# Optimization experiments

Measured on AMD Instinct MI355X. Metric: run time of the kernel, lower is better.

Reference implementation:

```python
import jax, jax.numpy as jnp
import numpy as np

NEG_SLOPE = 0.01
H = 128  # hidden_conv_1 == hidden_conv_2


def leaky(x):
    return jnp.where(x >= 0, x, NEG_SLOPE * x)


def gru_cell(x, h, w_ih, w_hh, b_ih, b_hh):
    # PyTorch GRUCell: gates stacked [r, z, n] along dim 0 of w_ih/w_hh
    gi = x @ w_ih.T + b_ih  # [N, 3H]
    gh = h @ w_hh.T + b_hh
    ir, iz, inn = jnp.split(gi, 3, axis=-1)
    hr, hz, hn = jnp.split(gh, 3, axis=-1)
    r = jax.nn.sigmoid(ir + hr)
    z = jax.nn.sigmoid(iz + hz)
    n = jnp.tanh(inn + r * hn)
    return (1.0 - z) * n + z * h


def gcn_conv(x, w, b, src, dst, num_nodes):
    # PyG GCNConv: add self-loops, symmetric normalization, linear first
    xw = x @ w.T  # [N, H]
    loop = jnp.arange(num_nodes, dtype=src.dtype)
    s = jnp.concatenate([src, loop])
    d = jnp.concatenate([dst, loop])
    deg = jax.ops.segment_sum(jnp.ones_like(d, dtype=x.dtype), d, num_segments=num_nodes)
    dinv = jnp.where(deg > 0, jax.lax.rsqrt(deg), 0.0)
    norm = dinv[s] * dinv[d]  # [E+N]
    msg = xw[s] * norm[:, None]
    out = jax.ops.segment_sum(msg, d, num_segments=num_nodes)
    return out + b


def setup_inputs() -> dict:
    key = jax.random.key(0)
    ks = jax.random.split(key, 24)
    N, E, EL, IN_DIM, OUT_DIM = 100000, 600000, 200000, 128, 2

    def lin(k, fan_in, fan_out):
        k1, k2 = jax.random.split(k)
        bound = 1.0 / np.sqrt(fan_in)
        w = jax.random.uniform(k1, (fan_out, fan_in), minval=-bound, maxval=bound, dtype=jnp.float32)
        b = jax.random.uniform(k2, (fan_out,), minval=-bound, maxval=bound, dtype=jnp.float32)
        return w, b

    w_pre1, b_pre1 = lin(ks[0], IN_DIM, 256)
    w_pre2, b_pre2 = lin(ks[1], 256, H)
    w_c1, b_c1 = lin(ks[2], H, H)
    w_c2, b_c2 = lin(ks[3], H, H)
    w_post, b_post = lin(ks[4], H, OUT_DIM)

    def gru_params(k):
        k1, k2, k3, k4 = jax.random.split(k, 4)
        bound = 1.0 / np.sqrt(H)
        u = lambda kk, shape: jax.random.uniform(kk, shape, minval=-bound, maxval=bound, dtype=jnp.float32)
        return u(k1, (3 * H, H)), u(k2, (3 * H, H)), u(k3, (3 * H,)), u(k4, (3 * H,))

    g1_wih, g1_whh, g1_bih, g1_bhh = gru_params(ks[5])
    g2_wih, g2_whh, g2_bih, g2_bhh = gru_params(ks[6])

    x = jax.random.normal(ks[7], (N, IN_DIM), dtype=jnp.float32)
    edge_index = jax.random.randint(ks[8], (2, E), 0, N, dtype=jnp.int64 if jax.config.jax_enable_x64 else jnp.int32)
    edge_label_index = jax.random.randint(ks[9], (2, EL), 0, N, dtype=edge_index.dtype)
    prev_emb0 = jax.random.normal(ks[10], (N, H), dtype=jnp.float32)
    prev_emb1 = jax.random.normal(ks[11], (N, H), dtype=jnp.float32)

    return {
        'x': x, 'edge_index': edge_index, 'edge_label_index': edge_label_index,
        'prev_emb0': prev_emb0, 'prev_emb1': prev_emb1,
        'w_pre1': w_pre1, 'b_pre1': b_pre1, 'w_pre2': w_pre2, 'b_pre2': b_pre2,
        'w_c1': w_c1, 'b_c1': b_c1, 'w_c2': w_c2, 'b_c2': b_c2,
        'w_post': w_post, 'b_post': b_post,
        'g1_wih': g1_wih, 'g1_whh': g1_whh, 'g1_bih': g1_bih, 'g1_bhh': g1_bhh,
        'g2_wih': g2_wih, 'g2_whh': g2_whh, 'g2_bih': g2_bih, 'g2_bhh': g2_bhh,
    }


def reference(x, edge_index, edge_label_index, prev_emb0, prev_emb1,
              w_pre1, b_pre1, w_pre2, b_pre2, w_c1, b_c1, w_c2, b_c2,
              w_post, b_post, g1_wih, g1_whh, g1_bih, g1_bhh,
              g2_wih, g2_whh, g2_bih, g2_bhh):
    N = x.shape[0]
    src, dst = edge_index[0], edge_index[1]

    # preprocess (dropout p=0.0 -> identity)
    h = leaky(x @ w_pre1.T + b_pre1)
    h = leaky(h @ w_pre2.T + b_pre2)

    # unconditional GRU fuse with previous 0-hop embedding (detached in torch)
    h = jax.lax.stop_gradient(gru_cell(h, prev_emb0, g1_wih, g1_whh, g1_bih, g1_bhh))
    emb0 = h

    h = leaky(gcn_conv(h, w_c1, b_c1, src, dst, N))
    h = jax.lax.stop_gradient(gru_cell(h, prev_emb0, g1_wih, g1_whh, g1_bih, g1_bhh))
    emb1 = h

    h = leaky(gcn_conv(h, w_c2, b_c2, src, dst, N))
    h = jax.lax.stop_gradient(gru_cell(h, prev_emb1, g2_wih, g2_whh, g2_bih, g2_bhh))
    emb2 = h

    # LP head: gather + hadamard + linear + sum
    h_src = h[edge_label_index[0]]
    h_dst = h[edge_label_index[1]]
    logits = jnp.sum((h_src * h_dst) @ w_post.T + b_post, axis=-1)  # [EL]
    return logits, emb0, emb1, emb2
```

## Files before the change

kernel.cpp:

```cpp
#include <hip/hip_runtime.h>
#include <hip/hip_bf16.h>
#include <type_traits>


typedef __bf16 bf16;
typedef __bf16 bf16x8 __attribute__((ext_vector_type(8)));
typedef float  f32x4  __attribute__((ext_vector_type(4)));

#define DEV __device__ __forceinline__

DEV f32x4 mfma16(bf16x8 a, bf16x8 b, f32x4 c) {
    return __builtin_amdgcn_mfma_f32_16x16x32_bf16(a, b, c, 0, 0, 0);
}

DEV bf16x8 load_a8(const float* p) {
    f32x4 lo = *(const f32x4*)p;
    f32x4 hi = *(const f32x4*)(p + 4);
    bf16x8 v;
    v[0] = (bf16)lo[0]; v[1] = (bf16)lo[1]; v[2] = (bf16)lo[2]; v[3] = (bf16)lo[3];
    v[4] = (bf16)hi[0]; v[5] = (bf16)hi[1]; v[6] = (bf16)hi[2]; v[7] = (bf16)hi[3];
    return v;
}
DEV bf16x8 load_a8(const bf16* p) { return *(const bf16x8*)p; }

__global__ void cvt8_kernel(const float* s0, const float* s1, const float* s2, const float* s3,
                            const float* s4, const float* s5, const float* s6, const float* s7,
                            bf16* __restrict__ wb) {
    const int i = blockIdx.x * 256 + threadIdx.x;
    if (i >= 294912) return;
    float v;
    if      (i < 32768)  v = s0[i];
    else if (i < 65536)  v = s1[i - 32768];
    else if (i < 81920)  v = s2[i - 65536];
    else if (i < 98304)  v = s3[i - 81920];
    else if (i < 147456) v = s4[i - 98304];
    else if (i < 196608) v = s5[i - 147456];
    else if (i < 245760) v = s6[i - 196608];
    else                 v = s7[i - 245760];
    wb[i] = (bf16)v;
}

template<int Ci, int Co, bool ACT, bool BIAS, typename AT, typename OT>
__global__ __launch_bounds__(256) void gemm_kernel(
    const AT* __restrict__ A, const bf16* __restrict__ W,
    const float* __restrict__ bias, OT* __restrict__ C, int M)
{
    const int tid  = threadIdx.x;
    const int lane = tid & 63, w = tid >> 6;
    const int lr   = lane & 15, ko = lane >> 4;
    const int rbase = blockIdx.x * 128 + w * 32;

    constexpr int KC = Ci / 32;
    constexpr int NT = Co / 16;

    bf16x8 a[2][KC];
#pragma unroll
    for (int m = 0; m < 2; ++m) {
        long arow = rbase + m * 16 + lr; if (arow > M - 1) arow = M - 1;
#pragma unroll
        for (int kc = 0; kc < KC; ++kc)
            a[m][kc] = load_a8(A + arow * Ci + kc * 32 + ko * 8);
    }

#pragma unroll
    for (int t = 0; t < NT; ++t) {
        f32x4 acc0 = {0.f, 0.f, 0.f, 0.f};
        f32x4 acc1 = {0.f, 0.f, 0.f, 0.f};
        const bf16* wp = W + (long)(t * 16 + lr) * Ci + ko * 8;
#pragma unroll
        for (int kc = 0; kc < KC; ++kc) {
            bf16x8 wf = *(const bf16x8*)(wp + kc * 32);
            acc0 = mfma16(a[0][kc], wf, acc0);
            acc1 = mfma16(a[1][kc], wf, acc1);
        }

        const int col = t * 16 + lr;
        float bv = 0.f;
        if (BIAS) bv = bias[col];
#pragma unroll
        for (int j = 0; j < 4; ++j) {
            const int r0 = rbase + ko * 4 + j;
            if (r0 < M) {
                float v = acc0[j] + bv;
                if (ACT) v = (v >= 0.f) ? v : 0.01f * v;
                C[(long)r0 * Co + col] = (OT)v;
            }
            const int r1 = rbase + 16 + ko * 4 + j;
            if (r1 < M) {
                float v = acc1[j] + bv;
                if (ACT) v = (v >= 0.f) ? v : 0.01f * v;
                C[(long)r1 * Co + col] = (OT)v;
            }
        }
    }
}

template<typename XT>
__global__ __launch_bounds__(256) void gru_kernel(
    const XT* x, const float* __restrict__ hp,
    const bf16* __restrict__ wih, const bf16* __restrict__ whh,
    const float* __restrict__ bih, const float* __restrict__ bhh,
    float* out, int N)
{
    __shared__ bf16 Lw[6][16][128];

    const int tid  = threadIdx.x;
    const int lane = tid & 63, w = tid >> 6;
    const int lr   = lane & 15, ko = lane >> 4;
    const long rbase = (long)blockIdx.x * 64 + w * 16;

    long arow = rbase + lr; if (arow > N - 1) arow = N - 1;
    bf16x8 ax[4], ah[4];
#pragma unroll
    for (int kc = 0; kc < 4; ++kc) {
        ax[kc] = load_a8(x  + arow * 128 + kc * 32 + ko * 8);
        ah[kc] = load_a8(hp + arow * 128 + kc * 32 + ko * 8);
    }

    bf16x8 pre[6];
    auto LDW = [&](int tc) {
#pragma unroll
        for (int i = 0; i < 6; ++i) {
            const int ch  = tid + 256 * i;
            const int g   = ch >> 8, rem = ch & 255;
            const int row = rem >> 4, cc = rem & 15;
            const int scc = cc ^ (row & 7);
            pre[i] = *(const bf16x8*)((g < 3 ? wih : whh)
                + (long)(((g % 3) * 128 + tc * 16 + row) * 128 + scc * 8));
        }
    };
    LDW(0);

    for (int tc = 0; tc < 8; ++tc) {
        __syncthreads();
#pragma unroll
        for (int i = 0; i < 6; ++i) {
            const int ch  = tid + 256 * i;
            const int g   = ch >> 8, rem = ch & 255;
            const int row = rem >> 4, cc = rem & 15;
            *(bf16x8*)(&Lw[g][row][cc * 8]) = pre[i];
        }
        __syncthreads();
        if (tc < 7) LDW(tc + 1);

        const int col = tc * 16 + lr;
        const float br = bih[col]       + bhh[col];
        const float bz = bih[128 + col] + bhh[128 + col];
        const float bi = bih[256 + col];
        const float bh = bhh[256 + col];

        f32x4 ar = {0.f, 0.f, 0.f, 0.f};
        f32x4 az = {0.f, 0.f, 0.f, 0.f};
        f32x4 ai = {0.f, 0.f, 0.f, 0.f};
        f32x4 ag = {0.f, 0.f, 0.f, 0.f};
#pragma unroll
        for (int kc = 0; kc < 4; ++kc) {
            const int cc = (kc * 4 + ko) ^ (lr & 7);
            bf16x8 wr_i = *(const bf16x8*)(&Lw[0][lr][cc * 8]);
            bf16x8 wz_i = *(const bf16x8*)(&Lw[1][lr][cc * 8]);
            bf16x8 wn_i = *(const bf16x8*)(&Lw[2][lr][cc * 8]);
            bf16x8 wr_h = *(const bf16x8*)(&Lw[3][lr][cc * 8]);
            bf16x8 wz_h = *(const bf16x8*)(&Lw[4][lr][cc * 8]);
            bf16x8 wn_h = *(const bf16x8*)(&Lw[5][lr][cc * 8]);
            ar = mfma16(ax[kc], wr_i, ar);
            ar = mfma16(ah[kc], wr_h, ar);
            az = mfma16(ax[kc], wz_i, az);
            az = mfma16(ah[kc], wz_h, az);
            ai = mfma16(ax[kc], wn_i, ai);
            ag = mfma16(ah[kc], wn_h, ag);
        }
#pragma unroll
        for (int j = 0; j < 4; ++j) {
            const long row = rbase + ko * 4 + j;
            if (row < N) {
                const float r = 1.f / (1.f + __expf(-(ar[j] + br)));
                const float z = 1.f / (1.f + __expf(-(az[j] + bz)));
                const float pre_ = (ai[j] + bi) + r * (ag[j] + bh);
                const float n = 1.f - 2.f / (1.f + __expf(2.f * pre_));
                out[row * 128 + col] = (1.f - z) * n + z * hp[row * 128 + col];
            }
        }
    }
}

__global__ __launch_bounds__(256) void gg_kernel(
    const bf16* __restrict__ xwb,
    const int* __restrict__ rowptr, const int* __restrict__ degi,
    const int* __restrict__ csr_src, const float* __restrict__ csr_norm,
    const float* __restrict__ dinv, const float* __restrict__ cbias,
    const float* __restrict__ hp,
    const bf16* __restrict__ wih, const bf16* __restrict__ whh,
    const float* __restrict__ bih, const float* __restrict__ bhh,
    float* __restrict__ out, int N)
{
    __shared__ bf16 Lw[6][16][128];

    const int tid  = threadIdx.x;
    const int lane = tid & 63, w = tid >> 6;
    const int lr   = lane & 15, ko = lane >> 4;
    const long rbase = (long)blockIdx.x * 64 + w * 16;

    long arow = rbase + lr; if (arow > N - 1) arow = N - 1;

    float acc[4][8];
#pragma unroll
    for (int kc = 0; kc < 4; ++kc)
#pragma unroll
        for (int j = 0; j < 8; ++j) acc[kc][j] = 0.f;
    {
        const int start = rowptr[arow];
        const int deg   = degi[arow];
        const bf16* xb  = xwb + ko * 8;
        for (int k = 0; k < deg; ++k) {
            const int   s  = csr_src[start + k];
            const float nm = csr_norm[start + k];
            const bf16* vp = xb + (long)s * 128;
            bf16x8 v0 = *(const bf16x8*)(vp);
            bf16x8 v1 = *(const bf16x8*)(vp + 32);
            bf16x8 v2 = *(const bf16x8*)(vp + 64);
            bf16x8 v3 = *(const bf16x8*)(vp + 96);
#pragma unroll
            for (int j = 0; j < 8; ++j) {
                acc[0][j] += (float)v0[j] * nm;
                acc[1][j] += (float)v1[j] * nm;
                acc[2][j] += (float)v2[j] * nm;
                acc[3][j] += (float)v3[j] * nm;
            }
        }
    }

    bf16x8 ax[4], ah[4];
    {
        const float di = dinv[arow], sl = di * di;
        const bf16* vp = xwb + (long)arow * 128 + ko * 8;
#pragma unroll
        for (int kc = 0; kc < 4; ++kc) {
            bf16x8 vd = *(const bf16x8*)(vp + kc * 32);
#pragma unroll
            for (int j = 0; j < 8; ++j) {
                float t = acc[kc][j] + (float)vd[j] * sl + cbias[kc * 32 + ko * 8 + j];
                t = (t >= 0.f) ? t : 0.01f * t;
                ax[kc][j] = (bf16)t;
            }
            ah[kc] = load_a8(hp + arow * 128 + kc * 32 + ko * 8);
        }
    }

    bf16x8 pre[6];
    auto LDW = [&](int tc) {
#pragma unroll
        for (int i = 0; i < 6; ++i) {
            const int ch  = tid + 256 * i;
            const int g   = ch >> 8, rem = ch & 255;
            const int row = rem >> 4, cc = rem & 15;
            const int scc = cc ^ (row & 7);
            pre[i] = *(const bf16x8*)((g < 3 ? wih : whh)
                + (long)(((g % 3) * 128 + tc * 16 + row) * 128 + scc * 8));
        }
    };
    LDW(0);

    for (int tc = 0; tc < 8; ++tc) {
        __syncthreads();
#pragma unroll
        for (int i = 0; i < 6; ++i) {
            const int ch  = tid + 256 * i;
            const int g   = ch >> 8, rem = ch & 255;
            const int row = rem >> 4, cc = rem & 15;
            *(bf16x8*)(&Lw[g][row][cc * 8]) = pre[i];
        }
        __syncthreads();
        if (tc < 7) LDW(tc + 1);

        const int col = tc * 16 + lr;
        const float br = bih[col]       + bhh[col];
        const float bz = bih[128 + col] + bhh[128 + col];
        const float bi = bih[256 + col];
        const float bh = bhh[256 + col];

        f32x4 ar = {0.f, 0.f, 0.f, 0.f};
        f32x4 az = {0.f, 0.f, 0.f, 0.f};
        f32x4 ai = {0.f, 0.f, 0.f, 0.f};
        f32x4 ag = {0.f, 0.f, 0.f, 0.f};
#pragma unroll
        for (int kc = 0; kc < 4; ++kc) {
            const int cc = (kc * 4 + ko) ^ (lr & 7);
            bf16x8 wr_i = *(const bf16x8*)(&Lw[0][lr][cc * 8]);
            bf16x8 wz_i = *(const bf16x8*)(&Lw[1][lr][cc * 8]);
            bf16x8 wn_i = *(const bf16x8*)(&Lw[2][lr][cc * 8]);
            bf16x8 wr_h = *(const bf16x8*)(&Lw[3][lr][cc * 8]);
            bf16x8 wz_h = *(const bf16x8*)(&Lw[4][lr][cc * 8]);
            bf16x8 wn_h = *(const bf16x8*)(&Lw[5][lr][cc * 8]);
            ar = mfma16(ax[kc], wr_i, ar);
            ar = mfma16(ah[kc], wr_h, ar);
            az = mfma16(ax[kc], wz_i, az);
            az = mfma16(ah[kc], wz_h, az);
            ai = mfma16(ax[kc], wn_i, ai);
            ag = mfma16(ah[kc], wn_h, ag);
        }
#pragma unroll
        for (int j = 0; j < 4; ++j) {
            const long row = rbase + ko * 4 + j;
            if (row < N) {
                const float r = 1.f / (1.f + __expf(-(ar[j] + br)));
                const float z = 1.f / (1.f + __expf(-(az[j] + bz)));
                const float pre_ = (ai[j] + bi) + r * (ag[j] + bh);
                const float n = 1.f - 2.f / (1.f + __expf(2.f * pre_));
                out[row * 128 + col] = (1.f - z) * n + z * hp[row * 128 + col];
            }
        }
    }
}

__global__ void deg_kernel(const int* __restrict__ dst, int* degi, int E) {
    const int e = blockIdx.x * 256 + threadIdx.x;
    if (e < E) atomicAdd(&degi[dst[e]], 1);
}
__global__ void scan1_kernel(const int* __restrict__ degi, int* __restrict__ inc,
                             int* __restrict__ bsum, float* __restrict__ dinv, int N) {
    __shared__ int s[256];
    const int i = blockIdx.x * 256 + threadIdx.x;
    const int d = (i < N) ? degi[i] : 0;
    if (i < N) dinv[i] = rsqrtf((float)d + 1.0f);
    s[threadIdx.x] = d;
    __syncthreads();
#pragma unroll
    for (int off = 1; off < 256; off <<= 1) {
        int t = (threadIdx.x >= off) ? s[threadIdx.x - off] : 0;
        __syncthreads();
        s[threadIdx.x] += t;
        __syncthreads();
    }
    if (i < N) inc[i] = s[threadIdx.x];
    if (threadIdx.x == 255) bsum[blockIdx.x] = s[255];
}
__global__ void scan2_kernel(int* bsum, int nb) {
    __shared__ int s[512];
    __shared__ int carry;
    if (threadIdx.x == 0) carry = 0;
    __syncthreads();
    for (int base = 0; base < nb; base += 512) {
        const int i = base + threadIdx.x;
        s[threadIdx.x] = (i < nb) ? bsum[i] : 0;
        __syncthreads();
#pragma unroll
        for (int off = 1; off < 512; off <<= 1) {
            int t = (threadIdx.x >= off) ? s[threadIdx.x - off] : 0;
            __syncthreads();
            s[threadIdx.x] += t;
            __syncthreads();
        }
        const int c = carry;
        if (i < nb) bsum[i] = s[threadIdx.x] + c;
        __syncthreads();
        if (threadIdx.x == 511) carry = c + s[511];
        __syncthreads();
    }
}
__global__ void scan3_kernel(const int* __restrict__ inc, const int* __restrict__ degi,
                             const int* __restrict__ bsum, int* __restrict__ rowptr,
                             int* __restrict__ rp2, int N) {
    const int i = blockIdx.x * 256 + threadIdx.x;
    if (i >= N) return;
    const int prev = (blockIdx.x > 0) ? bsum[blockIdx.x - 1] : 0;
    const int rp = prev + inc[i] - degi[i];
    rowptr[i] = rp;
    rp2[i]    = rp;
}
__global__ void fill_kernel(const int* __restrict__ src, const int* __restrict__ dst,
                            int* rp2, const float* __restrict__ dinv,
                            int* __restrict__ csr_src, float* __restrict__ csr_norm, int E) {
    const int e = blockIdx.x * 256 + threadIdx.x;
    if (e >= E) return;
    const int s = src[e], d = dst[e];
    const int pos = atomicAdd(&rp2[d], 1);
    csr_src[pos]  = s;
    csr_norm[pos] = dinv[s] * dinv[d];
}

template<typename OT>
__global__ __launch_bounds__(256) void gather_kernel(
    const bf16* __restrict__ xwb,
    const int* __restrict__ rowptr, const int* __restrict__ degi,
    const int* __restrict__ csr_src, const float* __restrict__ csr_norm,
    const float* __restrict__ dinv, const float* __restrict__ bias,
    OT* __restrict__ out, int N, int colbase, int cw, int lg)
{
    const long tid = (long)blockIdx.x * 256 + threadIdx.x;
    const long d = tid >> lg;
    const int  c = (int)(tid & ((1 << lg) - 1));
    if (d >= N) return;

    const int start = rowptr[d];
    const int deg   = degi[d];
    const int h     = deg >> 1;
    const bf16* xb  = xwb + c * 8;

    float acca[8] = {0.f, 0.f, 0.f, 0.f, 0.f, 0.f, 0.f, 0.f};
    float accb[8] = {0.f, 0.f, 0.f, 0.f, 0.f, 0.f, 0.f, 0.f};
    for (int k = 0; k < h; ++k) {
        const int   sa = csr_src[start + k];
        const int   sb = csr_src[start + h + k];
        const float na = csr_norm[start + k];
        const float nb_ = csr_norm[start + h + k];
        bf16x8 va = *(const bf16x8*)(xb + (long)sa * cw);
        bf16x8 vb = *(const bf16x8*)(xb + (long)sb * cw);
#pragma unroll
        for (int j = 0; j < 8; ++j) {
            acca[j] += (float)va[j] * na;
            accb[j] += (float)vb[j] * nb_;
        }
    }
    if (deg & 1) {
        const int   s  = csr_src[start + deg - 1];
        const float nm = csr_norm[start + deg - 1];
        bf16x8 v = *(const bf16x8*)(xb + (long)s * cw);
#pragma unroll
        for (int j = 0; j < 8; ++j) acca[j] += (float)v[j] * nm;
    }

    const float di = dinv[d], sl = di * di;
    bf16x8 vd = *(const bf16x8*)(xb + d * cw);
    const int col = colbase + c * 8;
    float v[8];
#pragma unroll
    for (int j = 0; j < 8; ++j) {
        float t = acca[j] + accb[j] + (float)vd[j] * sl + bias[col + j];
        v[j] = (t >= 0.f) ? t : 0.01f * t;
    }
    if constexpr (std::is_same<OT, bf16>::value) {
        bf16x8 o;
#pragma unroll
        for (int j = 0; j < 8; ++j) o[j] = (bf16)v[j];
        *(bf16x8*)(out + d * 128 + col) = o;
    } else {
        f32x4 o0, o1;
#pragma unroll
        for (int j = 0; j < 4; ++j) { o0[j] = v[j]; o1[j] = v[4 + j]; }
        *(f32x4*)(out + d * 128 + col)     = o0;
        *(f32x4*)(out + d * 128 + col + 4) = o1;
    }
}

__global__ __launch_bounds__(256) void lp_kernel(
    const float* __restrict__ emb, const int* __restrict__ eli,
    const float* __restrict__ wpost, const float* __restrict__ bpost,
    float* __restrict__ logits, int EL)
{
    const long t = (long)blockIdx.x * 256 + threadIdx.x;
    const long e = t >> 4;
    const int  c = (int)(t & 15);
    if (e >= EL) return;
    const long s = eli[e], d = eli[EL + e];

    f32x4 a0 = *(const f32x4*)(emb + s * 128 + c * 8);
    f32x4 a1 = *(const f32x4*)(emb + s * 128 + c * 8 + 4);
    f32x4 b0 = *(const f32x4*)(emb + d * 128 + c * 8);
    f32x4 b1 = *(const f32x4*)(emb + d * 128 + c * 8 + 4);
    f32x4 w00 = *(const f32x4*)(wpost + c * 8);
    f32x4 w01 = *(const f32x4*)(wpost + c * 8 + 4);
    f32x4 w10 = *(const f32x4*)(wpost + 128 + c * 8);
    f32x4 w11 = *(const f32x4*)(wpost + 128 + c * 8 + 4);

    float acc = 0.f;
#pragma unroll
    for (int i = 0; i < 4; ++i) {
        acc += a0[i] * b0[i] * (w00[i] + w10[i]);
        acc += a1[i] * b1[i] * (w01[i] + w11[i]);
    }
#pragma unroll
    for (int m = 1; m < 16; m <<= 1) acc += __shfl_xor(acc, m);
    if (c == 0) logits[e] = acc + bpost[0] + bpost[1];
}

extern "C" void kernel_launch(void* const* d_in, const int* in_sizes, int n_in,
                              void* d_out, int out_size, void* d_ws, size_t ws_size,
                              hipStream_t stream) {
    const float* x      = (const float*)d_in[0];
    const int*   ei     = (const int*)d_in[1];
    const int*   eli    = (const int*)d_in[2];
    const float* prev0  = (const float*)d_in[3];
    const float* prev1  = (const float*)d_in[4];
    const float* w_pre1 = (const float*)d_in[5];
    const float* b_pre1 = (const float*)d_in[6];
    const float* w_pre2 = (const float*)d_in[7];
    const float* b_pre2 = (const float*)d_in[8];
    const float* w_c1   = (const float*)d_in[9];
    const float* b_c1   = (const float*)d_in[10];
    const float* w_c2   = (const float*)d_in[11];
    const float* b_c2   = (const float*)d_in[12];
    const float* w_post = (const float*)d_in[13];
    const float* b_post = (const float*)d_in[14];
    const float* g1_wih = (const float*)d_in[15];
    const float* g1_whh = (const float*)d_in[16];
    const float* g1_bih = (const float*)d_in[17];
    const float* g1_bhh = (const float*)d_in[18];
    const float* g2_wih = (const float*)d_in[19];
    const float* g2_whh = (const float*)d_in[20];
    const float* g2_bih = (const float*)d_in[21];
    const float* g2_bhh = (const float*)d_in[22];

    const int N  = in_sizes[0] / 128;
    const int E  = in_sizes[1] / 2;
    const int EL = in_sizes[2] / 2;
    const long NH = (long)N * 128;

    float* out    = (float*)d_out;
    float* logits = out;
    float* emb0   = out + EL;
    float* emb1   = emb0 + NH;
    float* emb2   = emb1 + NH;

    bf16* H1b = (bf16*)emb1;
    bf16* H2b = (bf16*)emb2;
    bf16* h1b = (bf16*)emb2;

    char* ws = (char*)d_ws;
    size_t p = 0;
    auto alloc = [&](size_t bytes) { size_t o = p; p = (p + bytes + 255) & ~(size_t)255; return o; };
    float* dinv    = (float*)(ws + alloc((size_t)N * 4));
    int*   degi    = (int*)  (ws + alloc((size_t)N * 4));
    int*   inc     = (int*)  (ws + alloc((size_t)N * 4));
    int*   rowptr  = (int*)  (ws + alloc((size_t)N * 4));
    int*   rp2     = (int*)  (ws + alloc((size_t)N * 4));
    int*   bsum    = (int*)  (ws + alloc(4096));
    bf16*  wb      = (bf16*) (ws + alloc((size_t)294912 * 2));
    int*   csr_src = (int*)  (ws + alloc((size_t)E * 4));
    float* csr_nrm = (float*)(ws + alloc((size_t)E * 4));
    const size_t fixed = p;
    bf16*  xwb     = (bf16*)(ws + fixed);

    int cw = 128;
    while (cw > 16 && fixed + (size_t)N * cw * 2 > ws_size) cw >>= 1;
    const int lg = __builtin_ctz(cw >> 3);
    const int passes = 128 / cw;
    const bool fused = (cw == 128);
    const bool big_ws = fused &&
        (ws_size >= fixed + (size_t)N * 128 * 2 + (size_t)N * 128 * 2);
    bf16* h2b = big_ws ? (bf16*)(ws + fixed + (size_t)N * 128 * 2) : nullptr;

    bf16* wb_pre1 = wb;
    bf16* wb_pre2 = wb_pre1 + 32768;
    bf16* wb_c1   = wb_pre2 + 32768;
    bf16* wb_c2   = wb_c1 + 16384;
    bf16* wb_g1i  = wb_c2 + 16384;
    bf16* wb_g1h  = wb_g1i + 49152;
    bf16* wb_g2i  = wb_g1h + 49152;
    bf16* wb_g2h  = wb_g2i + 49152;

    const int gB = 256;
    const dim3 blk(gB);
    const int grid_rows128 = (N + 127) / 128;
    const int grid_gru     = (N + 63) / 64;
    const int grid_E       = (E + gB - 1) / gB;
    const int nb           = (N + 255) / 256;

    cvt8_kernel<<<(294912 + 255) / 256, blk, 0, stream>>>(
        w_pre1, w_pre2, w_c1, w_c2, g1_wih, g1_whh, g2_wih, g2_whh, wb);

    hipMemsetAsync(degi, 0, (size_t)N * 4, stream);
    deg_kernel<<<grid_E, blk, 0, stream>>>(ei + E, degi, E);
    scan1_kernel<<<nb, blk, 0, stream>>>(degi, inc, bsum, dinv, N);
    scan2_kernel<<<1, 512, 0, stream>>>(bsum, nb);
    scan3_kernel<<<nb, blk, 0, stream>>>(inc, degi, bsum, rowptr, rp2, N);
    fill_kernel<<<grid_E, blk, 0, stream>>>(ei, ei + E, rp2, dinv, csr_src, csr_nrm, E);

    gemm_kernel<128, 256, true, true, float, bf16><<<grid_rows128, blk, 0, stream>>>(x, wb_pre1, b_pre1, H1b, N);
    gemm_kernel<256, 128, true, true, bf16,  bf16><<<grid_rows128, blk, 0, stream>>>(H1b, wb_pre2, b_pre2, H2b, N);

    gru_kernel<bf16><<<grid_gru, blk, 0, stream>>>(H2b, prev0, wb_g1i, wb_g1h, g1_bih, g1_bhh, emb0, N);

    auto run_gemm = [&](const float* hin, const bf16* wp) {
        switch (cw) {
        case 128: gemm_kernel<128, 128, false, false, float, bf16><<<grid_rows128, blk, 0, stream>>>(hin, wp, nullptr, xwb, N); break;
        case 64:  gemm_kernel<128, 64,  false, false, float, bf16><<<grid_rows128, blk, 0, stream>>>(hin, wp, nullptr, xwb, N); break;
        case 32:  gemm_kernel<128, 32,  false, false, float, bf16><<<grid_rows128, blk, 0, stream>>>(hin, wp, nullptr, xwb, N); break;
        default:  gemm_kernel<128, 16,  false, false, float, bf16><<<grid_rows128, blk, 0, stream>>>(hin, wp, nullptr, xwb, N); break;
        }
    };

    if (fused) {
        run_gemm(emb0, wb_c1);
        gg_kernel<<<grid_gru, blk, 0, stream>>>(xwb, rowptr, degi, csr_src, csr_nrm,
                                                dinv, b_c1, prev0,
                                                wb_g1i, wb_g1h, g1_bih, g1_bhh, emb1, N);
        run_gemm(emb1, wb_c2);
        gg_kernel<<<grid_gru, blk, 0, stream>>>(xwb, rowptr, degi, csr_src, csr_nrm,
                                                dinv, b_c2, prev1,
                                                wb_g2i, wb_g2h, g2_bih, g2_bhh, emb2, N);
    } else {
        const int grid_ga = (int)((((long)N << lg) + gB - 1) / gB);
        for (int ps = 0; ps < passes; ++ps) {
            run_gemm(emb0, wb_c1 + (size_t)(ps * cw) * 128);
            gather_kernel<bf16><<<grid_ga, blk, 0, stream>>>(xwb, rowptr, degi, csr_src, csr_nrm,
                                                             dinv, b_c1, h1b, N, ps * cw, cw, lg);
        }
        gru_kernel<bf16><<<grid_gru, blk, 0, stream>>>(h1b, prev0, wb_g1i, wb_g1h, g1_bih, g1_bhh, emb1, N);
        for (int ps = 0; ps < passes; ++ps) {
            run_gemm(emb1, wb_c2 + (size_t)(ps * cw) * 128);
            if (big_ws)
                gather_kernel<bf16><<<grid_ga, blk, 0, stream>>>(xwb, rowptr, degi, csr_src, csr_nrm,
                                                                 dinv, b_c2, h2b, N, ps * cw, cw, lg);
            else
                gather_kernel<float><<<grid_ga, blk, 0, stream>>>(xwb, rowptr, degi, csr_src, csr_nrm,
                                                                  dinv, b_c2, emb2, N, ps * cw, cw, lg);
        }
        if (big_ws)
            gru_kernel<bf16><<<grid_gru, blk, 0, stream>>>(h2b, prev1, wb_g2i, wb_g2h, g2_bih, g2_bhh, emb2, N);
        else
            gru_kernel<float><<<grid_gru, blk, 0, stream>>>(emb2, prev1, wb_g2i, wb_g2h, g2_bih, g2_bhh, emb2, N);
    }

    lp_kernel<<<(int)(((long)EL * 16 + gB - 1) / gB), blk, 0, stream>>>(emb2, eli, w_post, b_post, logits, EL);
}
```

Measured before the change: 533.9 us.

## Distribute block's CSR edges across all threads with LDS atomic accumulation

The fused gather+GRU kernel no longer gives each lane one destination row to walk serially over its neighbours. All 256 threads now share the block's contiguous edge range, one (edge, 16-byte chunk) pair per thread, and scatter into a shared float accumulator with LDS atomics. This needs a new csr_dst array written by the fill kernel and a rowptr[N] sentinel. The aim is to remove load imbalance and idle lanes from varying degrees, at the cost of LDS atomics, extra shared memory reused for the weight tiles, and extra global traffic for csr_dst.

```diff
diff --git a/kernel.cpp b/kernel.cpp
--- a/kernel.cpp
+++ b/kernel.cpp
@@ -185,64 +185,70 @@
 
 __global__ __launch_bounds__(256) void gg_kernel(
     const bf16* __restrict__ xwb,
-    const int* __restrict__ rowptr, const int* __restrict__ degi,
+    const int* __restrict__ rowptr,
     const int* __restrict__ csr_src, const float* __restrict__ csr_norm,
+    const int* __restrict__ csr_dst,
     const float* __restrict__ dinv, const float* __restrict__ cbias,
     const float* __restrict__ hp,
     const bf16* __restrict__ wih, const bf16* __restrict__ whh,
     const float* __restrict__ bih, const float* __restrict__ bhh,
     float* __restrict__ out, int N)
 {
-    __shared__ bf16 Lw[6][16][128];
+    __shared__ float hacc[64][132];
+    bf16* LwBuf = (bf16*)&hacc[0][0];
 
     const int tid  = threadIdx.x;
     const int lane = tid & 63, w = tid >> 6;
     const int lr   = lane & 15, ko = lane >> 4;
-    const long rbase = (long)blockIdx.x * 64 + w * 16;
-
-    long arow = rbase + lr; if (arow > N - 1) arow = N - 1;
-
-    float acc[4][8];
-#pragma unroll
-    for (int kc = 0; kc < 4; ++kc)
-#pragma unroll
-        for (int j = 0; j < 8; ++j) acc[kc][j] = 0.f;
+    const long rbase = (long)blockIdx.x * 64;
+    const long wrow0 = rbase + w * 16;
+
+    long arow = wrow0 + lr; if (arow > N - 1) arow = N - 1;
+    const int lrow = (int)(arow - rbase);
+
+    float* hf = &hacc[0][0];
+#pragma unroll
+    for (int i = 0; i < 33; ++i) hf[tid + 256 * i] = 0.f;
+
+    bf16x8 ah[4], vd[4];
+#pragma unroll
+    for (int kc = 0; kc < 4; ++kc) {
+        ah[kc] = load_a8(hp + arow * 128 + kc * 32 + ko * 8);
+        vd[kc] = *(const bf16x8*)(xwb + (long)arow * 128 + kc * 32 + ko * 8);
+    }
+    __syncthreads();
+
     {
-        const int start = rowptr[arow];
-        const int deg   = degi[arow];
-        const bf16* xb  = xwb + ko * 8;
-        for (int k = 0; k < deg; ++k) {
-            const int   s  = csr_src[start + k];
-            const float nm = csr_norm[start + k];
-            const bf16* vp = xb + (long)s * 128;
-            bf16x8 v0 = *(const bf16x8*)(vp);
-            bf16x8 v1 = *(const bf16x8*)(vp + 32);
-            bf16x8 v2 = *(const bf16x8*)(vp + 64);
-            bf16x8 v3 = *(const bf16x8*)(vp + 96);
-#pragma unroll
-            for (int j = 0; j < 8; ++j) {
-                acc[0][j] += (float)v0[j] * nm;
-                acc[1][j] += (float)v1[j] * nm;
-                acc[2][j] += (float)v2[j] * nm;
-                acc[3][j] += (float)v3[j] * nm;
-            }
-        }
-    }
-
-    bf16x8 ax[4], ah[4];
+        const int estart = rowptr[rbase];
+        long rend = rbase + 64; if (rend > N) rend = N;
+        const int eend = rowptr[rend];
+        const int npair = (eend - estart) << 4;
+        for (int pi = tid; pi < npair; pi += 256) {
+            const int e = estart + (pi >> 4);
+            const int c = pi & 15;
+            const int   s  = csr_src[e];
+            const float nm = csr_norm[e];
+            const int   r  = csr_dst[e] - (int)rbase;
+            bf16x8 v = *(const bf16x8*)(xwb + (long)s * 128 + c * 8);
+            float* hq = &hacc[r][c * 8];
+#pragma unroll
+            for (int j = 0; j < 8; ++j) atomicAdd(hq + j, (float)v[j] * nm);
+        }
+    }
+    __syncthreads();
+
+    bf16x8 ax[4];
     {
         const float di = dinv[arow], sl = di * di;
-        const bf16* vp = xwb + (long)arow * 128 + ko * 8;
 #pragma unroll
         for (int kc = 0; kc < 4; ++kc) {
-            bf16x8 vd = *(const bf16x8*)(vp + kc * 32);
+            const int c0 = kc * 32 + ko * 8;
 #pragma unroll
             for (int j = 0; j < 8; ++j) {
-                float t = acc[kc][j] + (float)vd[j] * sl + cbias[kc * 32 + ko * 8 + j];
+                float t = hacc[lrow][c0 + j] + (float)vd[kc][j] * sl + cbias[c0 + j];
                 t = (t >= 0.f) ? t : 0.01f * t;
                 ax[kc][j] = (bf16)t;
             }
-            ah[kc] = load_a8(hp + arow * 128 + kc * 32 + ko * 8);
         }
     }
 
@@ -267,7 +273,7 @@
             const int ch  = tid + 256 * i;
             const int g   = ch >> 8, rem = ch & 255;
             const int row = rem >> 4, cc = rem & 15;
-            *(bf16x8*)(&Lw[g][row][cc * 8]) = pre[i];
+            *(bf16x8*)(LwBuf + g * 2048 + row * 128 + cc * 8) = pre[i];
         }
         __syncthreads();
         if (tc < 7) LDW(tc + 1);
@@ -285,12 +291,12 @@
 #pragma unroll
         for (int kc = 0; kc < 4; ++kc) {
             const int cc = (kc * 4 + ko) ^ (lr & 7);
-            bf16x8 wr_i = *(const bf16x8*)(&Lw[0][lr][cc * 8]);
-            bf16x8 wz_i = *(const bf16x8*)(&Lw[1][lr][cc * 8]);
-            bf16x8 wn_i = *(const bf16x8*)(&Lw[2][lr][cc * 8]);
-            bf16x8 wr_h = *(const bf16x8*)(&Lw[3][lr][cc * 8]);
-            bf16x8 wz_h = *(const bf16x8*)(&Lw[4][lr][cc * 8]);
-            bf16x8 wn_h = *(const bf16x8*)(&Lw[5][lr][cc * 8]);
+            bf16x8 wr_i = *(const bf16x8*)(LwBuf + 0 * 2048 + lr * 128 + cc * 8);
+            bf16x8 wz_i = *(const bf16x8*)(LwBuf + 1 * 2048 + lr * 128 + cc * 8);
+            bf16x8 wn_i = *(const bf16x8*)(LwBuf + 2 * 2048 + lr * 128 + cc * 8);
+            bf16x8 wr_h = *(const bf16x8*)(LwBuf + 3 * 2048 + lr * 128 + cc * 8);
+            bf16x8 wz_h = *(const bf16x8*)(LwBuf + 4 * 2048 + lr * 128 + cc * 8);
+            bf16x8 wn_h = *(const bf16x8*)(LwBuf + 5 * 2048 + lr * 128 + cc * 8);
             ar = mfma16(ax[kc], wr_i, ar);
             ar = mfma16(ah[kc], wr_h, ar);
             az = mfma16(ax[kc], wz_i, az);
@@ -300,7 +306,7 @@
         }
 #pragma unroll
         for (int j = 0; j < 4; ++j) {
-            const long row = rbase + ko * 4 + j;
+            const long row = wrow0 + ko * 4 + j;
             if (row < N) {
                 const float r = 1.f / (1.f + __expf(-(ar[j] + br)));
                 const float z = 1.f / (1.f + __expf(-(az[j] + bz)));
@@ -366,16 +372,19 @@
     const int rp = prev + inc[i] - degi[i];
     rowptr[i] = rp;
     rp2[i]    = rp;
+    if (i == N - 1) rowptr[N] = rp + degi[i];
 }
 __global__ void fill_kernel(const int* __restrict__ src, const int* __restrict__ dst,
                             int* rp2, const float* __restrict__ dinv,
-                            int* __restrict__ csr_src, float* __restrict__ csr_norm, int E) {
+                            int* __restrict__ csr_src, float* __restrict__ csr_norm,
+                            int* __restrict__ csr_dst, int E) {
     const int e = blockIdx.x * 256 + threadIdx.x;
     if (e >= E) return;
     const int s = src[e], d = dst[e];
     const int pos = atomicAdd(&rp2[d], 1);
     csr_src[pos]  = s;
     csr_norm[pos] = dinv[s] * dinv[d];
+    csr_dst[pos]  = d;
 }
 
 template<typename OT>
@@ -521,12 +530,13 @@
     float* dinv    = (float*)(ws + alloc((size_t)N * 4));
     int*   degi    = (int*)  (ws + alloc((size_t)N * 4));
     int*   inc     = (int*)  (ws + alloc((size_t)N * 4));
-    int*   rowptr  = (int*)  (ws + alloc((size_t)N * 4));
+    int*   rowptr  = (int*)  (ws + alloc((size_t)(N + 1) * 4));
     int*   rp2     = (int*)  (ws + alloc((size_t)N * 4));
     int*   bsum    = (int*)  (ws + alloc(4096));
     bf16*  wb      = (bf16*) (ws + alloc((size_t)294912 * 2));
     int*   csr_src = (int*)  (ws + alloc((size_t)E * 4));
     float* csr_nrm = (float*)(ws + alloc((size_t)E * 4));
+    int*   csr_dst = (int*)  (ws + alloc((size_t)E * 4));
     const size_t fixed = p;
     bf16*  xwb     = (bf16*)(ws + fixed);
 
@@ -563,7 +573,7 @@
     scan1_kernel<<<nb, blk, 0, stream>>>(degi, inc, bsum, dinv, N);
     scan2_kernel<<<1, 512, 0, stream>>>(bsum, nb);
     scan3_kernel<<<nb, blk, 0, stream>>>(inc, degi, bsum, rowptr, rp2, N);
-    fill_kernel<<<grid_E, blk, 0, stream>>>(ei, ei + E, rp2, dinv, csr_src, csr_nrm, E);
+    fill_kernel<<<grid_E, blk, 0, stream>>>(ei, ei + E, rp2, dinv, csr_src, csr_nrm, csr_dst, E);
 
     gemm_kernel<128, 256, true, true, float, bf16><<<grid_rows128, blk, 0, stream>>>(x, wb_pre1, b_pre1, H1b, N);
     gemm_kernel<256, 128, true, true, bf16,  bf16><<<grid_rows128, blk, 0, stream>>>(H1b, wb_pre2, b_pre2, H2b, N);
@@ -581,11 +591,11 @@
 
     if (fused) {
         run_gemm(emb0, wb_c1);
-        gg_kernel<<<grid_gru, blk, 0, stream>>>(xwb, rowptr, degi, csr_src, csr_nrm,
+        gg_kernel<<<grid_gru, blk, 0, stream>>>(xwb, rowptr, csr_src, csr_nrm, csr_dst,
                                                 dinv, b_c1, prev0,
                                                 wb_g1i, wb_g1h, g1_bih, g1_bhh, emb1, N);
         run_gemm(emb1, wb_c2);
-        gg_kernel<<<grid_gru, blk, 0, stream>>>(xwb, rowptr, degi, csr_src, csr_nrm,
+        gg_kernel<<<grid_gru, blk, 0, stream>>>(xwb, rowptr, csr_src, csr_nrm, csr_dst,
                                                 dinv, b_c2, prev1,
                                                 wb_g2i, wb_g2h, g2_bih, g2_bhh, emb2, N);
     } else {
```

Result: slower. 1.317 ms (+146.6%).

## Sort nodes by in-degree so fused gather-GRU waves have uniform trip counts

Applied to the files above, without the earlier changes.

Adds a degree histogram, scan and scatter that build a permutation of nodes bucketed by in-degree (capped at 63). The fused gather+GRU kernel then processes rows through this permutation, so lanes in a wavefront walk neighbor lists of similar length instead of waiting on the longest row. The cost is three extra small kernels plus a memset, indirect row indexing that scatters the output writes and hp reads, and loss of contiguous access to the prev-embedding rows.

```diff
diff --git a/kernel.cpp b/kernel.cpp
--- a/kernel.cpp
+++ b/kernel.cpp
@@ -187,6 +187,7 @@
     const bf16* __restrict__ xwb,
     const int* __restrict__ rowptr, const int* __restrict__ degi,
     const int* __restrict__ csr_src, const float* __restrict__ csr_norm,
+    const int* __restrict__ perm,
     const float* __restrict__ dinv, const float* __restrict__ cbias,
     const float* __restrict__ hp,
     const bf16* __restrict__ wih, const bf16* __restrict__ whh,
@@ -194,13 +195,21 @@
     float* __restrict__ out, int N)
 {
     __shared__ bf16 Lw[6][16][128];
+    __shared__ int  sperm[64];
 
     const int tid  = threadIdx.x;
     const int lane = tid & 63, w = tid >> 6;
     const int lr   = lane & 15, ko = lane >> 4;
-    const long rbase = (long)blockIdx.x * 64 + w * 16;
-
-    long arow = rbase + lr; if (arow > N - 1) arow = N - 1;
+    const long rbase = (long)blockIdx.x * 64;
+    const long wrow0 = rbase + w * 16;
+
+    if (tid < 64) {
+        long ii = rbase + tid; if (ii > N - 1) ii = N - 1;
+        sperm[tid] = perm[ii];
+    }
+    __syncthreads();
+
+    const long arow = sperm[w * 16 + lr];
 
     float acc[4][8];
 #pragma unroll
@@ -300,8 +309,8 @@
         }
 #pragma unroll
         for (int j = 0; j < 4; ++j) {
-            const long row = rbase + ko * 4 + j;
-            if (row < N) {
+            if (wrow0 + ko * 4 + j < N) {
+                const long row = sperm[w * 16 + ko * 4 + j];
                 const float r = 1.f / (1.f + __expf(-(ar[j] + br)));
                 const float z = 1.f / (1.f + __expf(-(az[j] + bz)));
                 const float pre_ = (ai[j] + bi) + r * (ag[j] + bh);
@@ -366,6 +375,7 @@
     const int rp = prev + inc[i] - degi[i];
     rowptr[i] = rp;
     rp2[i]    = rp;
+    if (i == N - 1) rowptr[N] = rp + degi[i];
 }
 __global__ void fill_kernel(const int* __restrict__ src, const int* __restrict__ dst,
                             int* rp2, const float* __restrict__ dinv,
@@ -376,6 +386,38 @@
     const int pos = atomicAdd(&rp2[d], 1);
     csr_src[pos]  = s;
     csr_norm[pos] = dinv[s] * dinv[d];
+}
+
+__global__ void dhist_kernel(const int* __restrict__ degi, int* dhist, int N) {
+    const int i = blockIdx.x * 256 + threadIdx.x;
+    if (i < N) {
+        int b = degi[i]; if (b > 63) b = 63;
+        atomicAdd(&dhist[b], 1);
+    }
+}
+__global__ void dscan_kernel(int* dhist) {
+    __shared__ int s[64];
+    const int t = threadIdx.x;
+    const int orig = dhist[t];
+    s[t] = orig;
+    __syncthreads();
+#pragma unroll
+    for (int off = 1; off < 64; off <<= 1) {
+        int v = (t >= off) ? s[t - off] : 0;
+        __syncthreads();
+        s[t] += v;
+        __syncthreads();
+    }
+    dhist[t] = s[t] - orig;
+}
+__global__ void dscatter_kernel(const int* __restrict__ degi, int* dhist,
+                                int* __restrict__ perm, int N) {
+    const int i = blockIdx.x * 256 + threadIdx.x;
+    if (i < N) {
+        int b = degi[i]; if (b > 63) b = 63;
+        const int pos = atomicAdd(&dhist[b], 1);
+        perm[pos] = i;
+    }
 }
 
 template<typename OT>
@@ -521,9 +563,11 @@
     float* dinv    = (float*)(ws + alloc((size_t)N * 4));
     int*   degi    = (int*)  (ws + alloc((size_t)N * 4));
     int*   inc     = (int*)  (ws + alloc((size_t)N * 4));
-    int*   rowptr  = (int*)  (ws + alloc((size_t)N * 4));
+    int*   rowptr  = (int*)  (ws + alloc((size_t)(N + 1) * 4));
     int*   rp2     = (int*)  (ws + alloc((size_t)N * 4));
+    int*   perm    = (int*)  (ws + alloc((size_t)N * 4));
     int*   bsum    = (int*)  (ws + alloc(4096));
+    int*   dhist   = (int*)  (ws + alloc(256));
     bf16*  wb      = (bf16*) (ws + alloc((size_t)294912 * 2));
     int*   csr_src = (int*)  (ws + alloc((size_t)E * 4));
     float* csr_nrm = (float*)(ws + alloc((size_t)E * 4));
@@ -553,6 +597,7 @@
     const int grid_rows128 = (N + 127) / 128;
     const int grid_gru     = (N + 63) / 64;
     const int grid_E       = (E + gB - 1) / gB;
+    const int grid_N       = (N + gB - 1) / gB;
     const int nb           = (N + 255) / 256;
 
     cvt8_kernel<<<(294912 + 255) / 256, blk, 0, stream>>>(
@@ -564,6 +609,10 @@
     scan2_kernel<<<1, 512, 0, stream>>>(bsum, nb);
     scan3_kernel<<<nb, blk, 0, stream>>>(inc, degi, bsum, rowptr, rp2, N);
     fill_kernel<<<grid_E, blk, 0, stream>>>(ei, ei + E, rp2, dinv, csr_src, csr_nrm, E);
+    hipMemsetAsync(dhist, 0, 256, stream);
+    dhist_kernel<<<grid_N, blk, 0, stream>>>(degi, dhist, N);
+    dscan_kernel<<<1, 64, 0, stream>>>(dhist);
+    dscatter_kernel<<<grid_N, blk, 0, stream>>>(degi, dhist, perm, N);
 
     gemm_kernel<128, 256, true, true, float, bf16><<<grid_rows128, blk, 0, stream>>>(x, wb_pre1, b_pre1, H1b, N);
     gemm_kernel<256, 128, true, true, bf16,  bf16><<<grid_rows128, blk, 0, stream>>>(H1b, wb_pre2, b_pre2, H2b, N);
@@ -581,11 +630,11 @@
 
     if (fused) {
         run_gemm(emb0, wb_c1);
-        gg_kernel<<<grid_gru, blk, 0, stream>>>(xwb, rowptr, degi, csr_src, csr_nrm,
+        gg_kernel<<<grid_gru, blk, 0, stream>>>(xwb, rowptr, degi, csr_src, csr_nrm, perm,
                                                 dinv, b_c1, prev0,
                                                 wb_g1i, wb_g1h, g1_bih, g1_bhh, emb1, N);
         run_gemm(emb1, wb_c2);
-        gg_kernel<<<grid_gru, blk, 0, stream>>>(xwb, rowptr, degi, csr_src, csr_nrm,
+        gg_kernel<<<grid_gru, blk, 0, stream>>>(xwb, rowptr, degi, csr_src, csr_nrm, perm,
                                                 dinv, b_c2, prev1,
                                                 wb_g2i, wb_g2h, g2_bih, g2_bhh, emb2, N);
     } else {
```

Result: slower. 1.287 ms (+141.0%).
